# Kernel optimization log

Measured on AMD Instinct MI355X. Metric: run time of the kernel, lower is better.

The kernel has to match this reference:

```python
import jax, jax.numpy as jnp
import numpy as np

W_IMG, H_IMG = 800.0, 600.0          # BoxList.size (w, h)
BBOX_W = (10.0, 10.0, 5.0, 5.0)      # BoxCoder weights
BBOX_CLAMP = float(np.log(1000.0 / 16.0))
SCORE_THRESH = 0.05
NMS_THRESH = 0.5
TOPN_PER_CLS = 300
DET_PER_IMG = 100


def setup_inputs() -> dict:
    key = jax.random.key(0)
    kl, kb, kp, kf = jax.random.split(key, 4)
    B, N, C, D = 2, 512, 151, 4096
    # spread logits so softmax produces scores above the 0.05 threshold
    class_logits = jax.random.normal(kl, (B, N, C), jnp.float32) * 4.0
    box_regression = jax.random.normal(kb, (B, N, C * 4), jnp.float32) * 0.2
    # valid xyxy proposal boxes inside the image
    pts = jax.random.uniform(kp, (B, N, 2, 2), jnp.float32)
    pts = pts * jnp.array([W_IMG - 1.0, H_IMG - 1.0], jnp.float32)
    lo = jnp.min(pts, axis=2)
    hi = jnp.max(pts, axis=2)
    proposal_boxes = jnp.concatenate([lo, hi], axis=-1)
    features = jax.random.normal(kf, (B, N, D), jnp.float32)
    return {"class_logits": class_logits, "box_regression": box_regression,
            "proposal_boxes": proposal_boxes, "features": features}


def decode_boxes(reg, boxes):
    wx, wy, ww, wh = BBOX_W
    widths = boxes[..., 2] - boxes[..., 0] + 1.0
    heights = boxes[..., 3] - boxes[..., 1] + 1.0
    ctr_x = boxes[..., 0] + 0.5 * widths
    ctr_y = boxes[..., 1] + 0.5 * heights
    dx = reg[..., 0] / wx
    dy = reg[..., 1] / wy
    dw = jnp.minimum(reg[..., 2] / ww, BBOX_CLAMP)
    dh = jnp.minimum(reg[..., 3] / wh, BBOX_CLAMP)
    pcx = dx * widths[..., None] + ctr_x[..., None]
    pcy = dy * heights[..., None] + ctr_y[..., None]
    pw = jnp.exp(dw) * widths[..., None]
    ph = jnp.exp(dh) * heights[..., None]
    return jnp.stack([pcx - 0.5 * pw, pcy - 0.5 * ph,
                      pcx + 0.5 * pw - 1.0, pcy + 0.5 * ph - 1.0], axis=-1)


def pairwise_iou(b):
    area = (b[:, 2] - b[:, 0] + 1.0) * (b[:, 3] - b[:, 1] + 1.0)
    xx1 = jnp.maximum(b[:, None, 0], b[None, :, 0])
    yy1 = jnp.maximum(b[:, None, 1], b[None, :, 1])
    xx2 = jnp.minimum(b[:, None, 2], b[None, :, 2])
    yy2 = jnp.minimum(b[:, None, 3], b[None, :, 3])
    inter = jnp.maximum(xx2 - xx1 + 1.0, 0.0) * jnp.maximum(yy2 - yy1 + 1.0, 0.0)
    return inter / (area[:, None] + area[None, :] - inter)


def class_nms(boxes, scores, valid):
    # Greedy NMS over one class of one image; fixed-shape, returns keep mask in
    # the ORIGINAL proposal order. `valid` = score > SCORE_THRESH prefilter.
    N = scores.shape[0]
    order = jnp.argsort(-scores)
    b = jax.lax.stop_gradient(boxes[order])
    v = valid[order]
    iou = pairwise_iou(b)
    idx = jnp.arange(N)
    def body(i, keep):
        sup = (iou[i] > NMS_THRESH) & (idx > i) & keep[i]
        return keep & ~sup
    keep = jax.lax.fori_loop(0, N, body, v)
    keep = keep & (jnp.cumsum(keep) <= TOPN_PER_CLS)  # post-NMS per-class top-n
    return jnp.zeros(N, bool).at[order].set(keep)


def reference(class_logits, box_regression, proposal_boxes, features):
    B, N, C = class_logits.shape
    prob = jax.nn.softmax(class_logits, axis=-1)                 # [B,N,C]
    reg = box_regression.reshape(B, N, C, 4)
    boxes = decode_boxes(reg, proposal_boxes)                    # [B,N,C,4]
    # clip_to_image(remove_empty=False)
    x = jnp.clip(boxes[..., 0::2], 0.0, W_IMG - 1.0)
    y = jnp.clip(boxes[..., 1::2], 0.0, H_IMG - 1.0)
    boxes = jnp.stack([x[..., 0], y[..., 0], x[..., 1], y[..., 1]], axis=-1)
    valid = prob > SCORE_THRESH                                  # [B,N,C]
    # per-(image, class) NMS, vectorized via vmap
    boxes_c = jnp.swapaxes(boxes, 1, 2)                          # [B,C,N,4]
    scores_c = jnp.swapaxes(prob, 1, 2)                          # [B,C,N]
    valid_c = jnp.swapaxes(valid, 1, 2)
    keep_c = jax.vmap(jax.vmap(class_nms))(boxes_c, scores_c, valid_c)
    keep = jnp.swapaxes(keep_c, 1, 2)                            # [B,N,C]
    keep = keep & (jnp.arange(C)[None, None, :] != 0)            # drop background
    # nms_filter_duplicates: one (score, label) per proposal
    dist_scores = prob * keep
    labels = jnp.argmax(dist_scores, axis=-1)                    # [B,N]
    scores_pre = jnp.max(dist_scores, axis=-1)                   # [B,N]
    det_valid = scores_pre > 0
    # detections_per_img cap via kth-largest threshold (only if over the cap)
    num = jnp.sum(det_valid, axis=-1)                            # [B]
    kth = jax.lax.top_k(jnp.where(det_valid, scores_pre, -1.0), DET_PER_IMG)[0][:, -1]
    thr = jnp.where(num > DET_PER_IMG, kth, -1.0)
    det_valid = det_valid & (scores_pre >= thr[:, None])
    # gather box of the winning class: boxes_per_cls[final_inds, labels_pre]
    final_boxes = jnp.take_along_axis(boxes, labels[..., None, None], axis=2)[:, :, 0, :]
    final_boxes = jnp.where(det_valid[..., None], final_boxes, 0.0)
    final_scores = jnp.where(det_valid, scores_pre, 0.0)
    final_labels = jnp.where(det_valid, labels, 0)
    nms_features = features * det_valid[..., None]               # features[orig_inds]
    return final_boxes, final_scores, final_labels, det_valid, nms_features
```

## Files before the change

kernel.cpp:

```cpp
#include <hip/hip_runtime.h>
#include <math.h>

#define Bn 2
#define Nn 512
#define Cn 151
#define Dn 4096
#define W_IMG 800.0f
#define H_IMG 600.0f
#define SCORE_T 0.05f
#define NMS_T 0.5f
#define TOPN 300
#define DETMAX 100
#define BBOX_CLAMP 4.135166556742356f
#define NBLK 256

#define OFF_BOXES  ((size_t)0)
#define OFF_SCORES ((size_t)(Bn * Nn * 4))
#define OFF_LABELS (OFF_SCORES + (size_t)(Bn * Nn))
#define OFF_VALID  (OFF_LABELS + (size_t)(Bn * Nn))
#define OFF_FEATS  (OFF_VALID + (size_t)(Bn * Nn))

__device__ __forceinline__ float4 decode_clip(const float4 pr, const float4 rg) {
  const float w = pr.z - pr.x + 1.0f;
  const float h = pr.w - pr.y + 1.0f;
  const float cx = pr.x + 0.5f * w;
  const float cy = pr.y + 0.5f * h;
  const float dx = rg.x / 10.0f;
  const float dy = rg.y / 10.0f;
  const float dw = fminf(rg.z / 5.0f, BBOX_CLAMP);
  const float dh = fminf(rg.w / 5.0f, BBOX_CLAMP);
  const float pcx = dx * w + cx;
  const float pcy = dy * h + cy;
  const float pw = expf(dw) * w;
  const float ph = expf(dh) * h;
  float x1 = pcx - 0.5f * pw;
  float y1 = pcy - 0.5f * ph;
  float x2 = pcx + 0.5f * pw - 1.0f;
  float y2 = pcy + 0.5f * ph - 1.0f;
  x1 = fminf(fmaxf(x1, 0.0f), W_IMG - 1.0f);
  x2 = fminf(fmaxf(x2, 0.0f), W_IMG - 1.0f);
  y1 = fminf(fmaxf(y1, 0.0f), H_IMG - 1.0f);
  y2 = fminf(fmaxf(y2, 0.0f), H_IMG - 1.0f);
  return make_float4(x1, y1, x2, y2);
}

__device__ __forceinline__ void grid_barrier(unsigned* arrive, unsigned* release,
                                             unsigned phase) {
  __syncthreads();
  if (threadIdx.x == 0) {
    __threadfence();
    atomicExch(&arrive[blockIdx.x], phase);
  }
  if (blockIdx.x == 0) {
    const unsigned j = threadIdx.x;
    while (atomicAdd(&arrive[j], 0u) != phase) __builtin_amdgcn_s_sleep(1);
    __syncthreads();
    if (threadIdx.x == 0) atomicExch(release, phase);
  }
  if (threadIdx.x == 0) {
    while (atomicAdd(release, 0u) != phase) __builtin_amdgcn_s_sleep(1);
    __threadfence();
  }
  __syncthreads();
}

struct FallbackWS {
  float fs[Nn];
  int   fn[Nn];
  float fb[Nn][4];
  unsigned char kp[Nn];
};
union SharedU {
  FallbackWS fwb[2];
  struct { unsigned hist[256]; int red[256]; unsigned dsel[2]; } p3;
};

__global__ __launch_bounds__(256, 1) void fused_kernel(
    const float* __restrict__ logits, const float* __restrict__ reg,
    const float* __restrict__ props, const float* __restrict__ feats,
    float* __restrict__ out,
    unsigned long long* __restrict__ packed, float* __restrict__ prob_t,
    unsigned* arrive, unsigned* release, float* __restrict__ thr) {
  __shared__ SharedU sh;
  const int blk = blockIdx.x;
  const int tid = threadIdx.x;
  const int wave = tid >> 6;
  const int lane = tid & 63;

  {
    const int bn = wave * NBLK + blk;
    const int b = bn >> 9;
    const int n = bn & (Nn - 1);
    const float* lrow = logits + (size_t)bn * Cn;
    const float l0 = lrow[lane];
    const float l1 = lrow[lane + 64];
    const float l2 = (lane + 128 < Cn) ? lrow[lane + 128] : -INFINITY;
    float mx = fmaxf(l0, fmaxf(l1, l2));
    #pragma unroll
    for (int o = 32; o > 0; o >>= 1) mx = fmaxf(mx, __shfl_xor(mx, o));
    const float e0 = expf(l0 - mx);
    const float e1 = expf(l1 - mx);
    const float e2 = (lane + 128 < Cn) ? expf(l2 - mx) : 0.0f;
    float sum = e0 + e1 + e2;
    #pragma unroll
    for (int o = 32; o > 0; o >>= 1) sum += __shfl_xor(sum, o);
    const float inv = 1.0f / sum;
    float* pt = prob_t + (size_t)b * Cn * Nn + n;
    pt[(size_t)lane * Nn] = e0 * inv;
    pt[(size_t)(lane + 64) * Nn] = e1 * inv;
    if (lane + 128 < Cn) pt[(size_t)(lane + 128) * Nn] = e2 * inv;
    if (lane == 0) packed[bn] = 0ull;
  }
  grid_barrier(arrive, release, 1u);

  {
    const int bc = wave * NBLK + blk;
    if (bc < Bn * Cn && (bc % Cn) != 0) {
      const int b = bc / Cn;
      const int c = bc % Cn;
      const float* col = prob_t + ((size_t)b * Cn + c) * Nn;

      float s_acc = -1.0f; int n_acc = -1;
      int base = 0;
      #pragma unroll
      for (int j = 0; j < Nn / 64; ++j) {
        const int n = j * 64 + lane;
        const float sv = col[n];
        const bool v = sv > SCORE_T;
        const unsigned long long m = __ballot(v);
        const int cnt = __popcll(m);
        if (cnt) {
          const int pos = base + __popcll(m & ((1ull << lane) - 1ull));
          const int dest = v ? (pos & 63) : 63;
          const int rs = __builtin_amdgcn_ds_permute(dest << 2, __float_as_int(sv));
          const int rn = __builtin_amdgcn_ds_permute(dest << 2, n);
          if (lane >= base && lane < base + cnt) { s_acc = __int_as_float(rs); n_acc = rn; }
          base += cnt;
        }
      }
      const int M = base;

      if (M > 0 && M < 64) {
        const float s = s_acc; const int n = n_acc;
        int rank = 0;
        for (int j = 0; j < M; ++j) {
          const float sj = __shfl(s, j);
          const int nj = __shfl(n, j);
          rank += ((sj > s) || (sj == s && nj < n)) ? 1 : 0;
        }
        const int rs2 = __builtin_amdgcn_ds_permute((rank & 63) << 2, __float_as_int(s));
        const int rn2 = __builtin_amdgcn_ds_permute((rank & 63) << 2, n);
        const float sc = __int_as_float(rs2);
        const int sn = rn2;
        float x1 = 0.0f, y1 = 0.0f, x2 = 0.0f, y2 = 0.0f;
        if (lane < M) {
          const int i = b * Nn + sn;
          const float4 pr = ((const float4*)props)[i];
          const float4 rg = ((const float4*)reg)[(size_t)i * Cn + c];
          const float4 bx = decode_clip(pr, rg);
          x1 = bx.x; y1 = bx.y; x2 = bx.z; y2 = bx.w;
        }
        const float area = (x2 - x1 + 1.0f) * (y2 - y1 + 1.0f);
        unsigned long long live = (1ull << M) - 1ull;
        int i = 0;
        while (i < 64) {
          const unsigned long long rem = live & (~0ull << i);
          if (!rem) break;
          i = __ffsll(rem) - 1;
          const float ax1 = __shfl(x1, i), ay1 = __shfl(y1, i);
          const float ax2 = __shfl(x2, i), ay2 = __shfl(y2, i);
          const float aarea = (ax2 - ax1 + 1.0f) * (ay2 - ay1 + 1.0f);
          const float xx1 = fmaxf(ax1, x1), yy1 = fmaxf(ay1, y1);
          const float xx2 = fminf(ax2, x2), yy2 = fminf(ay2, y2);
          const float inter = fmaxf(xx2 - xx1 + 1.0f, 0.0f) * fmaxf(yy2 - yy1 + 1.0f, 0.0f);
          const float iou = inter / (aarea + area - inter);
          const bool sup = (lane > i) && (lane < M) && ((live >> lane) & 1ull) && (iou > NMS_T);
          live &= ~__ballot(sup);
          ++i;
        }
        if (lane < M && ((live >> lane) & 1ull)) {
          const unsigned long long key =
              ((unsigned long long)__float_as_uint(sc) << 32) | (unsigned int)(Cn - c);
          atomicMax(&packed[(size_t)b * Nn + sn], key);
        }
      } else if (M >= 64) {
        FallbackWS* W = &sh.fwb[wave];
        int b2 = 0;
        for (int j = 0; j < Nn / 64; ++j) {
          const int n = j * 64 + lane;
          const float sv = col[n];
          const bool v = sv > SCORE_T;
          const unsigned long long m = __ballot(v);
          if (v) {
            const int pos = b2 + __popcll(m & ((1ull << lane) - 1ull));
            W->fb[pos][0] = sv;
            W->fb[pos][1] = __int_as_float(n);
          }
          b2 += __popcll(m);
        }
        __threadfence_block();
        for (int i0 = lane; i0 < M; i0 += 64) {
          const float si = W->fb[i0][0]; const int ni = __float_as_int(W->fb[i0][1]);
          int r = 0;
          for (int j = 0; j < M; ++j) {
            const float sj = W->fb[j][0]; const int nj = __float_as_int(W->fb[j][1]);
            r += ((sj > si) || (sj == si && nj < ni)) ? 1 : 0;
          }
          W->fs[r] = si; W->fn[r] = ni;
        }
        __threadfence_block();
        for (int i0 = lane; i0 < M; i0 += 64) {
          const int i = b * Nn + W->fn[i0];
          const float4 pr = ((const float4*)props)[i];
          const float4 rg = ((const float4*)reg)[(size_t)i * Cn + c];
          const float4 bx = decode_clip(pr, rg);
          W->fb[i0][0] = bx.x; W->fb[i0][1] = bx.y; W->fb[i0][2] = bx.z; W->fb[i0][3] = bx.w;
          W->kp[i0] = 1;
        }
        __threadfence_block();
        for (int i = 0; i < M; ++i) {
          if (!W->kp[i]) continue;
          const float ax1 = W->fb[i][0], ay1 = W->fb[i][1];
          const float ax2 = W->fb[i][2], ay2 = W->fb[i][3];
          const float aarea = (ax2 - ax1 + 1.0f) * (ay2 - ay1 + 1.0f);
          for (int t = i + 1 + lane; t < M; t += 64) {
            if (W->kp[t]) {
              const float bx1 = W->fb[t][0], by1 = W->fb[t][1];
              const float bx2 = W->fb[t][2], by2 = W->fb[t][3];
              const float barea = (bx2 - bx1 + 1.0f) * (by2 - by1 + 1.0f);
              const float xx1 = fmaxf(ax1, bx1), yy1 = fmaxf(ay1, by1);
              const float xx2 = fminf(ax2, bx2), yy2 = fminf(ay2, by2);
              const float inter = fmaxf(xx2 - xx1 + 1.0f, 0.0f) * fmaxf(yy2 - yy1 + 1.0f, 0.0f);
              if (inter / (aarea + barea - inter) > NMS_T) W->kp[t] = 0;
            }
          }
          __threadfence_block();
        }
        if (lane == 0) {
          int cnt = 0;
          for (int t = 0; t < M; ++t)
            if (W->kp[t]) { if (++cnt > TOPN) W->kp[t] = 0; }
        }
        __threadfence_block();
        for (int t = lane; t < M; t += 64) {
          if (W->kp[t]) {
            const unsigned long long key =
                ((unsigned long long)__float_as_uint(W->fs[t]) << 32) | (unsigned int)(Cn - c);
            atomicMax(&packed[(size_t)b * Nn + W->fn[t]], key);
          }
        }
      }
    }
  }
  grid_barrier(arrive, release, 2u);

  if (blk < Bn) {
    const int b = blk;
    const unsigned long long p0 = packed[(size_t)b * Nn + tid];
    const unsigned long long p1 = packed[(size_t)b * Nn + 256 + tid];
    const unsigned k0 = (unsigned)(p0 >> 32);
    const unsigned k1 = (unsigned)(p1 >> 32);
    sh.p3.red[tid] = (k0 ? 1 : 0) + (k1 ? 1 : 0);
    __syncthreads();
    for (int s2 = 128; s2 > 0; s2 >>= 1) {
      if (tid < s2) sh.p3.red[tid] += sh.p3.red[tid + s2];
      __syncthreads();
    }
    const int num = sh.p3.red[0];
    float tv = -1.0f;
    if (num > DETMAX) {
      unsigned prefix = 0;
      unsigned want = DETMAX;
      for (int shift = 24; shift >= 0; shift -= 8) {
        sh.p3.hist[tid] = 0;
        __syncthreads();
        const unsigned hm = (shift < 24) ? (0xFFFFFFFFu << (shift + 8)) : 0u;
        if (k0 && (k0 & hm) == (prefix & hm)) atomicAdd(&sh.p3.hist[(k0 >> shift) & 0xFF], 1u);
        if (k1 && (k1 & hm) == (prefix & hm)) atomicAdd(&sh.p3.hist[(k1 >> shift) & 0xFF], 1u);
        __syncthreads();
        if (tid < 64) {
          const int l = tid;
          const unsigned h0 = sh.p3.hist[4 * l], h1 = sh.p3.hist[4 * l + 1];
          const unsigned h2 = sh.p3.hist[4 * l + 2], h3 = sh.p3.hist[4 * l + 3];
          const unsigned chunk = h0 + h1 + h2 + h3;
          unsigned suf = chunk;
          #pragma unroll
          for (int off = 1; off < 64; off <<= 1) {
            const unsigned t2 = __shfl_down(suf, off);
            if (l + off < 64) suf += t2;
          }
          const unsigned g3 = suf - chunk;
          const unsigned g2 = g3 + h3;
          const unsigned g1 = g2 + h2;
          const unsigned g0 = g1 + h1;
          if (g3 < want && want <= g3 + h3) { sh.p3.dsel[0] = 4 * l + 3; sh.p3.dsel[1] = want - g3; }
          if (g2 < want && want <= g2 + h2) { sh.p3.dsel[0] = 4 * l + 2; sh.p3.dsel[1] = want - g2; }
          if (g1 < want && want <= g1 + h1) { sh.p3.dsel[0] = 4 * l + 1; sh.p3.dsel[1] = want - g1; }
          if (g0 < want && want <= g0 + h0) { sh.p3.dsel[0] = 4 * l + 0; sh.p3.dsel[1] = want - g0; }
        }
        __syncthreads();
        prefix |= sh.p3.dsel[0] << shift;
        want = sh.p3.dsel[1];
        __syncthreads();
      }
      tv = __uint_as_float(prefix);
    }
    if (tid == 0) thr[b] = tv;
  }
  grid_barrier(arrive, release, 3u);

  {
    const int row = blk * 4 + wave;
    const int b = row >> 9;
    const unsigned long long p = packed[row];
    const float s = __uint_as_float((unsigned)(p >> 32));
    const int label = (p != 0ull) ? (Cn - (int)(p & 0xFFFFFFFFull)) : 0;
    const float tb = thr[b];
    const bool valid = (s > 0.0f) && (s >= tb);
    if (lane == 0) {
      float4 ob = make_float4(0.0f, 0.0f, 0.0f, 0.0f);
      if (valid) {
        const float4 pr = ((const float4*)props)[row];
        const float4 rg = ((const float4*)reg)[(size_t)row * Cn + label];
        ob = decode_clip(pr, rg);
      }
      ((float4*)(out + OFF_BOXES))[row] = ob;
      out[OFF_SCORES + row] = valid ? s : 0.0f;
      out[OFF_LABELS + row] = valid ? (float)label : 0.0f;
      out[OFF_VALID + row] = valid ? 1.0f : 0.0f;
    }
    const float mval = valid ? 1.0f : 0.0f;
    const float4* fi = (const float4*)(feats + (size_t)row * Dn);
    float4* fo = (float4*)(out + OFF_FEATS + (size_t)row * Dn);
    #pragma unroll
    for (int i = 0; i < Dn / 4 / 64; ++i) {
      float4 x = fi[i * 64 + lane];
      x.x *= mval; x.y *= mval; x.z *= mval; x.w *= mval;
      fo[i * 64 + lane] = x;
    }
  }
}

extern "C" void kernel_launch(void* const* d_in, const int* in_sizes, int n_in,
                              void* d_out, int out_size, void* d_ws, size_t ws_size,
                              hipStream_t stream) {
  const float* logits = (const float*)d_in[0];
  const float* reg    = (const float*)d_in[1];
  const float* props  = (const float*)d_in[2];
  const float* feats  = (const float*)d_in[3];
  float* out = (float*)d_out;

  unsigned long long* packed = (unsigned long long*)d_ws;
  float* prob_t = (float*)(packed + Bn * Nn);
  unsigned* arrive = (unsigned*)(prob_t + (size_t)Bn * Cn * Nn);
  unsigned* release = arrive + NBLK;
  float* thr = (float*)(release + 1);

  fused_kernel<<<NBLK, 256, 0, stream>>>(logits, reg, props, feats, out,
                                         packed, prob_t, arrive, release, thr);
}
```

Measured before the change: 113.2 us.

## Drop final grid barrier by recomputing per-image threshold in every block

Every block now redundantly computes the detections-per-image radix-select threshold for both images into shared memory. This removes the last grid-wide barrier and the global threshold buffer. The barrier itself now uses padded arrive slots and atomic loads and stores with release semantics instead of atomicAdd/atomicExch polling. The cost is a small amount of duplicated reduction work in all 256 blocks.

```diff
diff --git a/kernel.cpp b/kernel.cpp
--- a/kernel.cpp
+++ b/kernel.cpp
@@ -44,21 +44,27 @@
   return make_float4(x1, y1, x2, y2);
 }
 
+#define ASTRIDE 16
 __device__ __forceinline__ void grid_barrier(unsigned* arrive, unsigned* release,
                                              unsigned phase) {
   __syncthreads();
   if (threadIdx.x == 0) {
     __threadfence();
-    atomicExch(&arrive[blockIdx.x], phase);
+    __hip_atomic_store(&arrive[blockIdx.x * ASTRIDE], phase,
+                       __ATOMIC_RELEASE, __HIP_MEMORY_SCOPE_AGENT);
   }
   if (blockIdx.x == 0) {
-    const unsigned j = threadIdx.x;
-    while (atomicAdd(&arrive[j], 0u) != phase) __builtin_amdgcn_s_sleep(1);
+    unsigned* slot = &arrive[threadIdx.x * ASTRIDE];
+    while (__hip_atomic_load(slot, __ATOMIC_RELAXED, __HIP_MEMORY_SCOPE_AGENT)
+           != phase) __builtin_amdgcn_s_sleep(1);
     __syncthreads();
-    if (threadIdx.x == 0) atomicExch(release, phase);
+    if (threadIdx.x == 0)
+      __hip_atomic_store(release, phase, __ATOMIC_RELEASE,
+                         __HIP_MEMORY_SCOPE_AGENT);
   }
   if (threadIdx.x == 0) {
-    while (atomicAdd(release, 0u) != phase) __builtin_amdgcn_s_sleep(1);
+    while (__hip_atomic_load(release, __ATOMIC_RELAXED, __HIP_MEMORY_SCOPE_AGENT)
+           != phase) __builtin_amdgcn_s_sleep(1);
     __threadfence();
   }
   __syncthreads();
@@ -80,8 +86,9 @@
     const float* __restrict__ props, const float* __restrict__ feats,
     float* __restrict__ out,
     unsigned long long* __restrict__ packed, float* __restrict__ prob_t,
-    unsigned* arrive, unsigned* release, float* __restrict__ thr) {
+    unsigned* arrive, unsigned* release) {
   __shared__ SharedU sh;
+  __shared__ float thrS[Bn];
   const int blk = blockIdx.x;
   const int tid = threadIdx.x;
   const int wave = tid >> 6;
@@ -254,12 +261,9 @@
   }
   grid_barrier(arrive, release, 2u);
 
-  if (blk < Bn) {
-    const int b = blk;
-    const unsigned long long p0 = packed[(size_t)b * Nn + tid];
-    const unsigned long long p1 = packed[(size_t)b * Nn + 256 + tid];
-    const unsigned k0 = (unsigned)(p0 >> 32);
-    const unsigned k1 = (unsigned)(p1 >> 32);
+  for (int b = 0; b < Bn; ++b) {
+    const unsigned k0 = (unsigned)(packed[(size_t)b * Nn + tid] >> 32);
+    const unsigned k1 = (unsigned)(packed[(size_t)b * Nn + 256 + tid] >> 32);
     sh.p3.red[tid] = (k0 ? 1 : 0) + (k1 ? 1 : 0);
     __syncthreads();
     for (int s2 = 128; s2 > 0; s2 >>= 1) {
@@ -267,6 +271,7 @@
       __syncthreads();
     }
     const int num = sh.p3.red[0];
+    __syncthreads();
     float tv = -1.0f;
     if (num > DETMAX) {
       unsigned prefix = 0;
@@ -305,9 +310,9 @@
       }
       tv = __uint_as_float(prefix);
     }
-    if (tid == 0) thr[b] = tv;
-  }
-  grid_barrier(arrive, release, 3u);
+    if (tid == 0) thrS[b] = tv;
+    __syncthreads();
+  }
 
   {
     const int row = blk * 4 + wave;
@@ -315,8 +320,7 @@
     const unsigned long long p = packed[row];
     const float s = __uint_as_float((unsigned)(p >> 32));
     const int label = (p != 0ull) ? (Cn - (int)(p & 0xFFFFFFFFull)) : 0;
-    const float tb = thr[b];
-    const bool valid = (s > 0.0f) && (s >= tb);
+    const bool valid = (s > 0.0f) && (s >= thrS[b]);
     if (lane == 0) {
       float4 ob = make_float4(0.0f, 0.0f, 0.0f, 0.0f);
       if (valid) {
@@ -353,9 +357,8 @@
   unsigned long long* packed = (unsigned long long*)d_ws;
   float* prob_t = (float*)(packed + Bn * Nn);
   unsigned* arrive = (unsigned*)(prob_t + (size_t)Bn * Cn * Nn);
-  unsigned* release = arrive + NBLK;
-  float* thr = (float*)(release + 1);
+  unsigned* release = arrive + NBLK * ASTRIDE;
 
   fused_kernel<<<NBLK, 256, 0, stream>>>(logits, reg, props, feats, out,
-                                         packed, prob_t, arrive, release, thr);
+                                         packed, prob_t, arrive, release);
 }
```

Measured after the change: 116.5 us. +2.8%, slower.
